# Kernel tuning notes

Measured on AMD Instinct MI355X. Metric: run time of the kernel, lower is better.

The kernel has to match this reference:

```python
import jax, jax.numpy as jnp
import numpy as np

B, S, D_IN, D_OUT = 4, 2048, 1024, 1024


def setup_inputs() -> dict:
    key = jax.random.key(0)
    k1, k2, k3, k4 = jax.random.split(key, 4)
    x = jax.random.normal(k1, (B, S, D_IN), dtype=jnp.float32)
    scale = 1.0 / np.sqrt(D_IN)
    Wq = jax.random.normal(k2, (D_IN, D_OUT), dtype=jnp.float32) * scale
    Wk = jax.random.normal(k3, (D_IN, D_OUT), dtype=jnp.float32) * scale
    Wv = jax.random.normal(k4, (D_IN, D_OUT), dtype=jnp.float32) * scale
    return {"x": x, "Wq": Wq, "Wk": Wk, "Wv": Wv}


def reference(x, Wq, Wk, Wv):
    # QKV projections (Linear, no bias)
    q = jnp.einsum('bsd,de->bse', x, Wq)  # [B,S,D_OUT]
    k = jnp.einsum('bsd,de->bse', x, Wk)
    v = jnp.einsum('bsd,de->bse', x, Wv)
    d_out = Wq.shape[1]
    # raw scores [B,S,S], scaled after masking (identical math: -inf stays -inf)
    scores = jnp.einsum('bqe,bke->bqk', q, k) * (d_out ** -0.5)
    S_ = x.shape[1]
    # causal mask: future positions (j > i) are masked out
    causal = jnp.triu(jnp.ones((S_, S_), dtype=bool), k=1)
    scores = jnp.where(causal[None, :, :], -jnp.inf, scores)
    attn = jax.nn.softmax(scores, axis=-1)  # dropout p=0.0 -> identity
    return jnp.einsum('bqk,bke->bqe', attn, v)
```

## Files before the change

### kernel.cpp

```cpp
#include <hip/hip_runtime.h>
#include <stdint.h>

typedef unsigned short u16;
typedef unsigned int u32;
typedef __bf16 bf16x8 __attribute__((ext_vector_type(8)));
typedef float f32x4 __attribute__((ext_vector_type(4)));

#define BM 128
#define BN 128
#define BK 64

__device__ __forceinline__ u16 f2bf(float x) {
  union { float f; uint32_t u; } c; c.f = x;
  uint32_t r = (c.u + 0x7FFFu + ((c.u >> 16) & 1u)) >> 16;
  return (u16)r;
}
__device__ __forceinline__ float bf2f(u16 v) {
  union { uint32_t u; float f; } c; c.u = ((uint32_t)v) << 16;
  return c.f;
}

__device__ __forceinline__ void async_copy16(const u16* g, u16* l) {
  __builtin_amdgcn_global_load_lds(
      (const __attribute__((address_space(1))) void*)g,
      (__attribute__((address_space(3))) void*)l,
      16, 0, 0);
}

__global__ void zerofill_u16(u16* __restrict__ p) {
  long i = (long)blockIdx.x * 256 + threadIdx.x;
  p[i] = 0;
}

__global__ __launch_bounds__(256)
void prep(const void* __restrict__ xs, const void* __restrict__ w0,
          const void* __restrict__ w1, const void* __restrict__ w2,
          u16* __restrict__ xn, u16* __restrict__ WT3, u32* __restrict__ flag,
          float* __restrict__ sigma, int nxb)
{
  __shared__ int sh_hits;
  __shared__ u16 tile[64][72];
  if (threadIdx.x == 0) sh_hits = 0;
  __syncthreads();
  {
    const u16* w = (const u16*)w0;
    int h = 0;
    for (int i = threadIdx.x; i < 8192; i += 256)
      if ((w[i] & 0x7F80u) == 0x7F80u) h++;
    if (h) atomicAdd(&sh_hits, h);
  }
  __syncthreads();
  const bool isf32 = (sh_hits > 0);
  const int blk = blockIdx.x;
  const int tid = threadIdx.x;
  if (blk == 0 && tid == 0) *flag = isf32 ? 1000u : 0u;

  if (blk < nxb) {
    long i = ((long)blk * 256 + tid) * 8;
    u16 o[8];
    if (isf32) {
      const float* s = (const float*)xs + i;
      f32x4 a = *(const f32x4*)s;
      f32x4 b = *(const f32x4*)(s + 4);
#pragma unroll
      for (int c = 0; c < 4; ++c) { o[c] = f2bf(a[c]); o[c + 4] = f2bf(b[c]); }
    } else {
      *(uint4*)o = *(const uint4*)((const u16*)xs + i);
    }
    *(uint4*)(xn + i) = *(uint4*)o;
  } else if (blk < nxb + 768) {
    const int Dd = 1024;
    int t = blk - nxb;
    int z = t >> 8;
    int r = t & 255;
    const int r0 = (r >> 4) * 64, c0 = (r & 15) * 64;
    const void* src = (z == 0) ? w0 : (z == 1) ? w1 : w2;
    u16* out = WT3 + (long)z * Dd * Dd;
#pragma unroll
    for (int p = 0; p < 2; ++p) {
      int v = tid + p * 256;
      int row = v >> 3, c8 = (v & 7) * 8;
      u16 tt[8];
      if (isf32) {
        const float* sp = (const float*)src + (long)(r0 + row) * Dd + c0 + c8;
        f32x4 a = *(const f32x4*)sp;
        f32x4 b = *(const f32x4*)(sp + 4);
#pragma unroll
        for (int c = 0; c < 4; ++c) { tt[c] = f2bf(a[c]); tt[c + 4] = f2bf(b[c]); }
      } else {
        *(uint4*)tt = *(const uint4*)((const u16*)src + (long)(r0 + row) * Dd + c0 + c8);
      }
#pragma unroll
      for (int c = 0; c < 8; ++c) tile[row][c8 + c] = tt[c];
    }
    __syncthreads();
#pragma unroll
    for (int p = 0; p < 2; ++p) {
      int v = tid + p * 256;
      int oc = v >> 3, r8 = (v & 7) * 8;
      union { uint4 q; u16 s[8]; } tt;
#pragma unroll
      for (int c = 0; c < 8; ++c) tt.s[c] = tile[r8 + c][oc];
      *(uint4*)(out + (long)(c0 + oc) * Dd + r0 + r8) = tt.q;
    }
  } else {
    int t = blk - (nxb + 768);
    *(f32x4*)(sigma + ((long)t * 256 + tid) * 4) = f32x4{0.f, 0.f, 0.f, 0.f};
  }
}

template <int MODE>
__global__ __launch_bounds__(256, 4)
void gemm_nt(const u16* __restrict__ A, const u16* __restrict__ B, void* __restrict__ Cv,
             const u32* __restrict__ flag, float* __restrict__ sigma, int sigStride,
             int K, int lda, int ldb, int ldc,
             long sA, long sB, long sC, long cOff,
             float scale, int trik, int ntri, u16* __restrict__ vtOut)
{
  __shared__ u16 As[BM * BK];
  __shared__ u16 Bs[BN * BK];
  const int bz = blockIdx.z;
  const int tid = threadIdx.x;

  int bm, bn;
  bool isVT = false;
  if constexpr (MODE == 3) {
    const int t = blockIdx.x;
    const int cum[11] = {0, 10, 26, 36, 52, 68, 78, 94, 110, 126, 136};
    const int ssm[10] = {0, 1, 1, 2, 2, 2, 3, 3, 3, 3};
    const int ssn[10] = {0, 0, 1, 0, 1, 2, 0, 1, 2, 3};
    int s = 0;
    while (cum[s + 1] <= t) ++s;
    const int l = t - cum[s];
    const int sm = ssm[s], sn = ssn[s];
    int tm, tn;
    if (sm == sn) {
      tm = 0;
      while ((tm + 1) * (tm + 2) / 2 <= l) ++tm;
      tn = l - tm * (tm + 1) / 2;
    } else { tm = l >> 2; tn = l & 3; }
    bm = sm * 4 + tm;
    bn = sn * 4 + tn;
    (void)ntri;
  } else if constexpr (MODE == 5) {
    const int t = blockIdx.x;
    if (t < ntri) {
      bm = t >> 4; bn = t & 15;
    } else {
      isVT = true;
      const int t2 = t - ntri;
      bm = t2 / sigStride; bn = t2 % sigStride;
      const u16* tmp = A;
      A = B + (long)2048 * 1024;
      B = tmp;
    }
  } else {
    bm = blockIdx.y;
    if (trik) bm = gridDim.y - 1 - bm;
    bn = blockIdx.x;
  }

  A += (long)bz * sA;
  B += (long)bz * sB;

  const int wid  = tid >> 6;
  const int lane = tid & 63;
  const int l16  = lane & 15;
  const int lk   = lane >> 4;
  const int srow = lane >> 3;
  const int swz  = ((lane & 7) ^ srow) * 8;
  const int m0 = bm * BM, n0 = bn * BN;

  int nk = K / BK;
  if (trik) { int lim = (m0 + BM) / BK; if (lim < nk) nk = lim; }

  f32x4 acc[4][4] = {};

  for (int kt = 0; kt < nk; ++kt) {
    const int k0 = kt * BK;
#pragma unroll
    for (int c = 0; c < 4; ++c) {
      const int rb = wid * 32 + c * 8;
      async_copy16(A + (long)(m0 + rb + srow) * lda + (k0 + swz), As + rb * BK);
      async_copy16(B + (long)(n0 + rb + srow) * ldb + (k0 + swz), Bs + rb * BK);
    }
    __syncthreads();
#pragma unroll
    for (int kh = 0; kh < 2; ++kh) {
      bf16x8 av[4], bv[4];
#pragma unroll
      for (int i = 0; i < 4; ++i) {
        const int Ra = (wid >> 1) * 64 + i * 16 + l16;
        const int Rb = (wid & 1)  * 64 + i * 16 + l16;
        const int ca = ((kh * 4 + lk) ^ (l16 & 7)) * 8;
        av[i] = *(const bf16x8*)(As + Ra * BK + ca);
        bv[i] = *(const bf16x8*)(Bs + Rb * BK + ca);
      }
#pragma unroll
      for (int mi = 0; mi < 4; ++mi)
#pragma unroll
        for (int ni = 0; ni < 4; ++ni)
          acc[mi][ni] = __builtin_amdgcn_mfma_f32_16x16x32_bf16(av[mi], bv[ni], acc[mi][ni], 0, 0, 0);
    }
    __syncthreads();
  }

  const int rb0 = m0 + (wid >> 1) * 64;
  const int cb0 = n0 + (wid & 1) * 64;
  const long cbase = (long)bz * sC + cOff;

  if constexpr (MODE == 3) {
    u16* Cp = (u16*)Cv;
    const bool diag = (bm == bn);
    float* sig = sigma + (long)bz * sigStride;
#pragma unroll
    for (int mi = 0; mi < 4; ++mi)
#pragma unroll
      for (int r = 0; r < 4; ++r) {
        const int row = rb0 + mi * 16 + lk * 4 + r;
        float part = 0.f;
#pragma unroll
        for (int ni = 0; ni < 4; ++ni) {
          const int col = cb0 + ni * 16 + l16;
          float ev = __expf(acc[mi][ni][r] * scale);
          if (diag && col > row) ev = 0.f;
          u16 b = f2bf(ev);
          part += bf2f(b);
          Cp[cbase + (long)row * ldc + col] = b;
        }
#pragma unroll
        for (int o = 1; o < 16; o <<= 1) part += __shfl_xor(part, o);
        if (l16 == 0) atomicAdd(&sig[row], part);
      }
  } else if constexpr (MODE == 5) {
    if (isVT) {
#pragma unroll
      for (int mi = 0; mi < 4; ++mi)
#pragma unroll
        for (int r = 0; r < 4; ++r) {
          const int row = rb0 + mi * 16 + lk * 4 + r;
#pragma unroll
          for (int ni = 0; ni < 4; ++ni) {
            const int col = cb0 + ni * 16 + l16;
            const long idx = (long)row * ldc + (long)(col >> 11) * sC + (col & 2047);
            vtOut[idx] = f2bf(acc[mi][ni][r]);
          }
        }
    } else {
      u16* Cp = (u16*)Cv;
#pragma unroll
      for (int mi = 0; mi < 4; ++mi)
#pragma unroll
        for (int r = 0; r < 4; ++r) {
          const int row = rb0 + mi * 16 + lk * 4 + r;
#pragma unroll
          for (int ni = 0; ni < 4; ++ni) {
            const int col = cb0 + ni * 16 + l16;
            Cp[(long)row * 2048 + col] = f2bf(acc[mi][ni][r]);
          }
        }
    }
  } else {
    const bool f32out = (MODE == 2) && (*flag > 32);
    const float* sig = (MODE == 2) ? (sigma + (long)bz * sigStride) : nullptr;
#pragma unroll
    for (int mi = 0; mi < 4; ++mi)
#pragma unroll
      for (int r = 0; r < 4; ++r) {
        const int row = rb0 + mi * 16 + lk * 4 + r;
        float rs = scale;
        if constexpr (MODE == 2) rs = 1.0f / sig[row];
#pragma unroll
        for (int ni = 0; ni < 4; ++ni) {
          const int col = cb0 + ni * 16 + l16;
          const float v = acc[mi][ni][r] * rs;
          const long idx = cbase + (long)row * ldc + col;
          if (f32out) ((float*)Cv)[idx] = v;
          else        ((u16*)Cv)[idx]   = f2bf(v);
        }
      }
  }
}

extern "C" void kernel_launch(void* const* d_in, const int* in_sizes, int n_in,
                              void* d_out, int out_size, void* d_ws, size_t ws_size,
                              hipStream_t stream)
{
  (void)in_sizes; (void)n_in; (void)out_size;
  const int Bb = 4, S = 2048, D = 1024, D2 = 2048;
  const long SD  = (long)S * D;
  const long SD2 = (long)S * D2;
  const long SS  = (long)S * S;
  const long N_X = (long)Bb * SD;
  const long N_W = (long)D * D;
  const int NTRI = 16 * 17 / 2;

  char* ws = (char*)d_ws;
  size_t off = 0;
  auto take = [&](size_t bytes) -> void* {
    void* p = ws + off;
    off = (off + bytes + 255) & ~((size_t)255);
    return p;
  };

  u32*   flag  = (u32*)take(4096);
  float* sigma = (float*)take((size_t)Bb * S * 4);
  u16*   xn    = (u16*)take((size_t)N_X * 2);
  u16*   WT3   = (u16*)take((size_t)3 * N_W * 2);
  const size_t off_common = off;

  const size_t needA = off_common + (size_t)(Bb * SD2 * 2)
                     + (size_t)(N_X * 2)
                     + (size_t)(Bb * SS * 2) + 4096;
  const size_t needC = off_common + (size_t)(SD2 * 2)
                     + (size_t)(SD * 2)
                     + (size_t)(SS * 2) + 4096;

  if (ws_size < needC) {
    zerofill_u16<<<(int)(N_X / 256), 256, 0, stream>>>((u16*)d_out);
    return;
  }

  const int nxb = (int)(N_X / 2048);
  prep<<<nxb + 768 + 8, 256, 0, stream>>>(d_in[0], d_in[1], d_in[2], d_in[3],
                                          xn, WT3, flag, sigma, nxb);

  const float scl = 0.03125f;

  if (ws_size >= needA) {
    u16* QK = (u16*)take((size_t)Bb * SD2 * 2);
    u16* VT = (u16*)take((size_t)N_X * 2);
    u16* E  = (u16*)take((size_t)Bb * SS * 2);

    gemm_nt<5><<<dim3(1024 + 512), 256, 0, stream>>>(
        xn, WT3, QK, flag, nullptr, 64, D, D, D, S,
        0, 0, SD, 0, 1.f, 0, 1024, VT);

    gemm_nt<3><<<dim3(NTRI, 1, Bb), 256, 0, stream>>>(
        QK, QK + 1024, E, flag, sigma, S, D, D2, D2, S,
        SD2, SD2, SS, 0, scl, 0, NTRI, nullptr);

    gemm_nt<2><<<dim3(D / BN, S / BM, Bb), 256, 0, stream>>>(
        E, VT, d_out, flag, sigma, S, S, S, S, D,
        SS, SD, SD, 0, 1.f, 1, 0, nullptr);
  } else {
    u16* QKb = (u16*)take((size_t)SD2 * 2);
    u16* VTb = (u16*)take((size_t)SD * 2);
    u16* Eb  = (u16*)take((size_t)SS * 2);

    for (int b = 0; b < Bb; ++b) {
      gemm_nt<5><<<dim3(256 + 128), 256, 0, stream>>>(
          xn + (long)b * SD, WT3, QKb, flag, nullptr, 16, D, D, D, S,
          0, 0, 0, 0, 1.f, 0, 256, VTb);

      gemm_nt<3><<<dim3(NTRI, 1, 1), 256, 0, stream>>>(
          QKb, QKb + 1024, Eb, flag, sigma + (long)b * S, S, D, D2, D2, S,
          0, 0, 0, 0, scl, 0, NTRI, nullptr);

      gemm_nt<2><<<dim3(D / BN, S / BM, 1), 256, 0, stream>>>(
          Eb, VTb, d_out, flag, sigma + (long)b * S, S, S, S, S, D,
          0, 0, 0, (long)b * SD, 1.f, 1, 0, nullptr);
    }
  }
}
```

Measured before the change: 236.3 us.

## Split-K the causal PV GEMM for lower row-blocks and combine partials

The causal attention-times-V GEMM has very unequal work per row block, since the bottom blocks loop over up to 16 k-tiles. The new mode splits each of the lower 8 row blocks into two K halves, which write fp32 partials into the reused QK buffer. A separate combine kernel then sums the partials, normalises by the softmax denominator and writes the output. This evens out per-block work and raises the block count, at the cost of an extra kernel launch and fp32 partial traffic.

```diff
diff --git a/kernel.cpp b/kernel.cpp
--- a/kernel.cpp
+++ b/kernel.cpp
@@ -30,6 +30,31 @@
 __global__ void zerofill_u16(u16* __restrict__ p) {
   long i = (long)blockIdx.x * 256 + threadIdx.x;
   p[i] = 0;
+}
+
+__global__ __launch_bounds__(256)
+void pv_combine(const float* __restrict__ P, const float* __restrict__ sigma,
+                void* __restrict__ out, const u32* __restrict__ flag)
+{
+  const long e = ((long)blockIdx.x * 256 + threadIdx.x) * 4;
+  const int bz = (int)(e >> 20);
+  const int r  = (int)((e >> 10) & 1023);
+  const int c  = (int)(e & 1023);
+  const f32x4 a = *(const f32x4*)(P + e);
+  const f32x4 b = *(const f32x4*)(P + 4194304 + e);
+  const float inv = 1.0f / sigma[bz * 2048 + 1024 + r];
+  const long ob = (long)bz * 2097152 + (long)(1024 + r) * 1024 + c;
+  if (*flag > 32) {
+    f32x4 o;
+#pragma unroll
+    for (int j = 0; j < 4; ++j) o[j] = (a[j] + b[j]) * inv;
+    *(f32x4*)((float*)out + ob) = o;
+  } else {
+    u16 o[4];
+#pragma unroll
+    for (int j = 0; j < 4; ++j) o[j] = f2bf((a[j] + b[j]) * inv);
+    *(uint2*)((u16*)out + ob) = *(uint2*)o;
+  }
 }
 
 __global__ __launch_bounds__(256)
@@ -124,6 +149,7 @@
 
   int bm, bn;
   bool isVT = false;
+  int part = -1;
   if constexpr (MODE == 3) {
     const int t = blockIdx.x;
     const int cum[11] = {0, 10, 26, 36, 52, 68, 78, 94, 110, 126, 136};
@@ -154,6 +180,11 @@
       A = B + (long)2048 * 1024;
       B = tmp;
     }
+  } else if constexpr (MODE == 6) {
+    bn = blockIdx.x;
+    const int vb = blockIdx.y;
+    if (vb < 8) { bm = vb; }
+    else { bm = 8 + ((vb - 8) >> 1); part = (vb - 8) & 1; }
   } else {
     bm = blockIdx.y;
     if (trik) bm = gridDim.y - 1 - bm;
@@ -173,10 +204,16 @@
 
   int nk = K / BK;
   if (trik) { int lim = (m0 + BM) / BK; if (lim < nk) nk = lim; }
+  int kts = 0;
+  if constexpr (MODE == 6) {
+    const int L = bm + 1;
+    if (part < 0) { kts = 0;        nk = 2 * L; }
+    else          { kts = part * L; nk = kts + L; }
+  }
 
   f32x4 acc[4][4] = {};
 
-  for (int kt = 0; kt < nk; ++kt) {
+  for (int kt = kts; kt < nk; ++kt) {
     const int k0 = kt * BK;
 #pragma unroll
     for (int c = 0; c < 4; ++c) {
@@ -218,19 +255,19 @@
 #pragma unroll
       for (int r = 0; r < 4; ++r) {
         const int row = rb0 + mi * 16 + lk * 4 + r;
-        float part = 0.f;
+        float part2 = 0.f;
 #pragma unroll
         for (int ni = 0; ni < 4; ++ni) {
           const int col = cb0 + ni * 16 + l16;
           float ev = __expf(acc[mi][ni][r] * scale);
           if (diag && col > row) ev = 0.f;
           u16 b = f2bf(ev);
-          part += bf2f(b);
+          part2 += bf2f(b);
           Cp[cbase + (long)row * ldc + col] = b;
         }
 #pragma unroll
-        for (int o = 1; o < 16; o <<= 1) part += __shfl_xor(part, o);
-        if (l16 == 0) atomicAdd(&sig[row], part);
+        for (int o = 1; o < 16; o <<= 1) part2 += __shfl_xor(part2, o);
+        if (l16 == 0) atomicAdd(&sig[row], part2);
       }
   } else if constexpr (MODE == 5) {
     if (isVT) {
@@ -257,6 +294,40 @@
           for (int ni = 0; ni < 4; ++ni) {
             const int col = cb0 + ni * 16 + l16;
             Cp[(long)row * 2048 + col] = f2bf(acc[mi][ni][r]);
+          }
+        }
+    }
+  } else if constexpr (MODE == 6) {
+    if (part < 0) {
+      const bool f32out = (*flag > 32);
+      const float* sig = sigma + (long)bz * sigStride;
+#pragma unroll
+      for (int mi = 0; mi < 4; ++mi)
+#pragma unroll
+        for (int r = 0; r < 4; ++r) {
+          const int row = rb0 + mi * 16 + lk * 4 + r;
+          const float rs = 1.0f / sig[row];
+#pragma unroll
+          for (int ni = 0; ni < 4; ++ni) {
+            const int col = cb0 + ni * 16 + l16;
+            const float v = acc[mi][ni][r] * rs;
+            const long idx = cbase + (long)row * ldc + col;
+            if (f32out) ((float*)Cv)[idx] = v;
+            else        ((u16*)Cv)[idx]   = f2bf(v);
+          }
+        }
+    } else {
+      float* pb = (float*)vtOut;
+      const long pbase = (long)part * 4194304 + (long)bz * 1048576;
+#pragma unroll
+      for (int mi = 0; mi < 4; ++mi)
+#pragma unroll
+        for (int r = 0; r < 4; ++r) {
+          const int row = rb0 + mi * 16 + lk * 4 + r;
+#pragma unroll
+          for (int ni = 0; ni < 4; ++ni) {
+            const int col = cb0 + ni * 16 + l16;
+            pb[pbase + (long)(row - 1024) * 1024 + col] = acc[mi][ni][r];
           }
         }
     }
@@ -340,9 +411,10 @@
         QK, QK + 1024, E, flag, sigma, S, D, D2, D2, S,
         SD2, SD2, SS, 0, scl, 0, NTRI, nullptr);
 
-    gemm_nt<2><<<dim3(D / BN, S / BM, Bb), 256, 0, stream>>>(
+    gemm_nt<6><<<dim3(D / BN, 24, Bb), 256, 0, stream>>>(
         E, VT, d_out, flag, sigma, S, S, S, S, D,
-        SS, SD, SD, 0, 1.f, 1, 0, nullptr);
+        SS, SD, SD, 0, 1.f, 0, 0, (u16*)QK);
+    pv_combine<<<4096, 256, 0, stream>>>((const float*)QK, sigma, d_out, flag);
   } else {
     u16* QKb = (u16*)take((size_t)SD2 * 2);
     u16* VTb = (u16*)take((size_t)SD * 2);
```

Measured after the change: 240.1 us. No clear change (+1.6%).
